# Performance work log

Measured on AMD Instinct MI355X. Metric: run time of the kernel, lower is better.

## Reference

```python
import jax, jax.numpy as jnp
import numpy as np

BATCH, BITS = 1024, 2048
STD = 0.01


def sine_act(x):
    # MySine: 0.5*(1+sin((x-0.5)*pi)), symmetric about 0.5
    return 0.5 * (1.0 + jnp.sin((x - 0.5) * jnp.pi))


def qubo_cost(xb, Q):
    # cost_fn_tensor: per-row QUBO cost c_i = x_i^T Q x_i  -> shape [batch]
    return jnp.einsum('bi,ij,bj->b', xb, Q, xb)


def setup_inputs() -> dict:
    key = jax.random.key(0)
    k1, k2, k3, k4, k5 = jax.random.split(key, 5)
    x = jax.random.uniform(k1, (BATCH, BITS), dtype=jnp.float32)
    noise = jax.random.uniform(k2, (BATCH, BITS), dtype=jnp.float32)  # rand_like in Sample_Binary
    # generate_weights_and_biases: W = I + N(0, std^2), b = N(0, std^2); fc2 gets identical values
    W1 = jnp.eye(BITS, dtype=jnp.float32) + STD * jax.random.normal(k3, (BITS, BITS), dtype=jnp.float32)
    b1 = STD * jax.random.normal(k4, (BITS,), dtype=jnp.float32)
    W2 = W1
    b2 = b1
    # concrete TSP-style QUBO cost matrix (baked into cost_fn in the original repo)
    Q = jax.random.normal(k5, (BITS, BITS), dtype=jnp.float32) / np.float32(BITS)
    return {"x": x, "noise": noise, "W1": W1, "b1": b1, "W2": W2, "b2": b2, "Q": Q}


def reference(x, noise, W1, b1, W2, b2, Q):
    # fc1 + MySine
    h = sine_act(x @ W1.T + b1)
    # fc2 + MySine (layers == 2)
    h = sine_act(h @ W2.T + b2)
    # Sample_Binary: straight-through Bernoulli sample
    sampled = (noise < h).astype(jnp.float32)
    xb = h + jax.lax.stop_gradient(sampled - h)  # numerically exactly 0/1
    # BinaryToCost forward: per-row cost
    return qubo_cost(xb, Q)
```

## Files before the change

### kernel.cpp

```cpp
#include <hip/hip_runtime.h>
#include <math.h>

#define BATCH 1024
#define BITS  2048

typedef __attribute__((ext_vector_type(8))) short bf16x8;
typedef __attribute__((ext_vector_type(4))) float f32x4;
typedef _Float16 f16_t;
typedef __attribute__((ext_vector_type(8))) _Float16 f16x8;

__device__ __constant__ double D_PI = 3.141592653589793;

static __device__ __forceinline__ unsigned short f32_to_bf16(float f) {
    unsigned int u = __float_as_uint(f);
    u += 0x7fffu + ((u >> 16) & 1u);
    return (unsigned short)(u >> 16);
}

__global__ __launch_bounds__(256)
void split_w(const float* __restrict__ W, f16_t* __restrict__ eh, f16_t* __restrict__ el)
{
    const size_t base = ((size_t)blockIdx.x * 256 + threadIdx.x) * 8;
    const int n = (int)(base >> 11);
    const int k0 = (int)(base & 2047);
    float4 w0 = *(const float4*)&W[base];
    float4 w1 = *(const float4*)&W[base + 4];
    float wv[8] = {w0.x, w0.y, w0.z, w0.w, w1.x, w1.y, w1.z, w1.w};
    f16x8 hv, lv;
    #pragma unroll
    for (int j = 0; j < 8; ++j) {
        float e = wv[j] - ((n == k0 + j) ? 1.0f : 0.0f);
        f16_t h = (f16_t)e;
        hv[j] = h;
        lv[j] = (f16_t)((e - (float)h) * 2048.0f);
    }
    *(f16x8*)&eh[base] = hv;
    *(f16x8*)&el[base] = lv;
}

__global__ __launch_bounds__(256)
void split_x(const float* __restrict__ X, f16_t* __restrict__ xh, f16_t* __restrict__ xl)
{
    const size_t base = ((size_t)blockIdx.x * 256 + threadIdx.x) * 8;
    float4 w0 = *(const float4*)&X[base];
    float4 w1 = *(const float4*)&X[base + 4];
    float wv[8] = {w0.x, w0.y, w0.z, w0.w, w1.x, w1.y, w1.z, w1.w};
    f16x8 hv, lv;
    #pragma unroll
    for (int j = 0; j < 8; ++j) {
        f16_t h = (f16_t)wv[j];
        hv[j] = h;
        lv[j] = (f16_t)((wv[j] - (float)h) * 2048.0f);
    }
    *(f16x8*)&xh[base] = hv;
    *(f16x8*)&xl[base] = lv;
}

#define LBM 64
#define LBN 64
#define LBK 64
#define LLS 72

__global__ __launch_bounds__(256)
void layer_mfma(const f16_t* __restrict__ Ah, const f16_t* __restrict__ Al,
                const f16_t* __restrict__ Ebh, const f16_t* __restrict__ Ebl,
                const float* __restrict__ direct, const float* __restrict__ bias,
                const float* __restrict__ noise,
                float* __restrict__ h_f32, f16_t* __restrict__ h_hi,
                f16_t* __restrict__ h_lo, unsigned short* __restrict__ xb_out,
                int mode)
{
    __shared__ __align__(16) f16_t sAh[LBM][LLS], sAl[LBM][LLS];
    __shared__ __align__(16) f16_t sEh[LBN][LLS], sEl[LBN][LLS];

    const int t = threadIdx.x;
    const int wave = t >> 6, lane = t & 63;
    const int quad = lane >> 4, li = lane & 15;
    const int mw = wave & 1, nw = wave >> 1;
    const int row0 = blockIdx.y * LBM, col0 = blockIdx.x * LBN;

    f32x4 acc[2][2][4];
    double acc64[2][2][4];
    #pragma unroll
    for (int tm = 0; tm < 2; ++tm)
        #pragma unroll
        for (int tn = 0; tn < 2; ++tn) {
            #pragma unroll
            for (int p = 0; p < 4; ++p) acc[tm][tn][p] = (f32x4){0.f,0.f,0.f,0.f};
            #pragma unroll
            for (int r = 0; r < 4; ++r) acc64[tm][tn][r] = 0.0;
        }

    const float C1 = 1.0f / 2048.0f;
    const float C2 = 1.0f / (2048.0f * 2048.0f);
    const int srow = t >> 2;
    const int sko  = (t & 3) * 16;

    for (int kt = 0; kt < BITS / LBK; ++kt) {
        const int k0 = kt * LBK;
        {
            const size_t ga = (size_t)(row0 + srow) * BITS + k0 + sko;
            const size_t ge = (size_t)(col0 + srow) * BITS + k0 + sko;
            *(f16x8*)&sAh[srow][sko]     = *(const f16x8*)&Ah[ga];
            *(f16x8*)&sAh[srow][sko + 8] = *(const f16x8*)&Ah[ga + 8];
            *(f16x8*)&sAl[srow][sko]     = *(const f16x8*)&Al[ga];
            *(f16x8*)&sAl[srow][sko + 8] = *(const f16x8*)&Al[ga + 8];
            *(f16x8*)&sEh[srow][sko]     = *(const f16x8*)&Ebh[ge];
            *(f16x8*)&sEh[srow][sko + 8] = *(const f16x8*)&Ebh[ge + 8];
            *(f16x8*)&sEl[srow][sko]     = *(const f16x8*)&Ebl[ge];
            *(f16x8*)&sEl[srow][sko + 8] = *(const f16x8*)&Ebl[ge + 8];
        }
        __syncthreads();

        #pragma unroll
        for (int ks = 0; ks < LBK; ks += 32) {
            f16x8 ah[2], al[2], bh[2], bl[2];
            #pragma unroll
            for (int tm = 0; tm < 2; ++tm) {
                const int r = mw * 32 + tm * 16 + li, c = ks + quad * 8;
                ah[tm] = *(const f16x8*)&sAh[r][c];
                al[tm] = *(const f16x8*)&sAl[r][c];
            }
            #pragma unroll
            for (int tn = 0; tn < 2; ++tn) {
                const int r = nw * 32 + tn * 16 + li, c = ks + quad * 8;
                bh[tn] = *(const f16x8*)&sEh[r][c];
                bl[tn] = *(const f16x8*)&sEl[r][c];
            }
            #pragma unroll
            for (int tm = 0; tm < 2; ++tm)
                #pragma unroll
                for (int tn = 0; tn < 2; ++tn) {
                    acc[tm][tn][0] = __builtin_amdgcn_mfma_f32_16x16x32_f16(ah[tm], bh[tn], acc[tm][tn][0], 0, 0, 0);
                    acc[tm][tn][1] = __builtin_amdgcn_mfma_f32_16x16x32_f16(ah[tm], bl[tn], acc[tm][tn][1], 0, 0, 0);
                    acc[tm][tn][2] = __builtin_amdgcn_mfma_f32_16x16x32_f16(al[tm], bh[tn], acc[tm][tn][2], 0, 0, 0);
                    acc[tm][tn][3] = __builtin_amdgcn_mfma_f32_16x16x32_f16(al[tm], bl[tn], acc[tm][tn][3], 0, 0, 0);
                }
        }
        __syncthreads();

        if ((kt & 7) == 7) {
            #pragma unroll
            for (int tm = 0; tm < 2; ++tm)
                #pragma unroll
                for (int tn = 0; tn < 2; ++tn) {
                    #pragma unroll
                    for (int r = 0; r < 4; ++r) {
                        float s = fmaf(C2, acc[tm][tn][3][r],
                                  fmaf(C1, acc[tm][tn][2][r],
                                  fmaf(C1, acc[tm][tn][1][r], acc[tm][tn][0][r])));
                        acc64[tm][tn][r] += (double)s;
                    }
                    #pragma unroll
                    for (int p = 0; p < 4; ++p) acc[tm][tn][p] = (f32x4){0.f,0.f,0.f,0.f};
                }
        }
    }

    #pragma unroll
    for (int tm = 0; tm < 2; ++tm)
        #pragma unroll
        for (int tn = 0; tn < 2; ++tn)
            #pragma unroll
            for (int r = 0; r < 4; ++r) {
                const int m = row0 + mw * 32 + tm * 16 + quad * 4 + r;
                const int n = col0 + nw * 32 + tn * 16 + li;
                const size_t idx = (size_t)m * BITS + n;
                double pre = acc64[tm][tn][r] + (double)direct[idx] + (double)bias[n];
                double h = 0.5 * (1.0 + sin((pre - 0.5) * D_PI));
                if (mode == 0) {
                    h_f32[idx] = (float)h;
                    f16_t hh = (f16_t)h;
                    h_hi[idx] = hh;
                    h_lo[idx] = (f16_t)((h - (double)hh) * 2048.0);
                } else {
                    xb_out[idx] = ((double)noise[idx] < h) ? (unsigned short)0x3F80
                                                           : (unsigned short)0;
                }
            }
}

__global__ __launch_bounds__(256)
void transpose_q(const float* __restrict__ Q, unsigned short* __restrict__ QT)
{
    __shared__ unsigned short tile[32][33];
    const int t = threadIdx.x;
    const int tx = t & 31, ty = t >> 5;
    const int i0 = blockIdx.y * 32, j0 = blockIdx.x * 32;
    #pragma unroll
    for (int r = 0; r < 4; ++r) {
        const int i = ty + r * 8;
        tile[i][tx] = f32_to_bf16(Q[(size_t)(i0 + i) * BITS + j0 + tx]);
    }
    __syncthreads();
    #pragma unroll
    for (int r = 0; r < 4; ++r) {
        const int j = ty + r * 8;
        QT[(size_t)(j0 + j) * BITS + i0 + tx] = tile[tx][j];
    }
}

#define CBM 64
#define CBN 128
#define CBK 64
#define LSTR (CBK + 8)

__global__ __launch_bounds__(256)
void cost_kernel(const unsigned short* __restrict__ xb,
                 const unsigned short* __restrict__ QT,
                 float* __restrict__ out)
{
    __shared__ unsigned short Ab[CBM][LSTR];
    __shared__ unsigned short Bb[CBN][LSTR];
    __shared__ float red[2][CBM][17];

    const int t = threadIdx.x;
    const int wave = t >> 6, lane = t & 63;
    const int quad = lane >> 4, li = lane & 15;
    const int mw = wave & 1, nw = wave >> 1;
    const int b0 = blockIdx.y * CBM, j0 = blockIdx.x * CBN;

    f32x4 acc[2][4];
    #pragma unroll
    for (int tm = 0; tm < 2; ++tm)
        #pragma unroll
        for (int tn = 0; tn < 4; ++tn)
            acc[tm][tn] = (f32x4){0.f, 0.f, 0.f, 0.f};

    for (int k0 = 0; k0 < BITS; k0 += CBK) {
        #pragma unroll
        for (int i = 0; i < 2; ++i) {
            const int c = t + 256 * i;
            const int row = c >> 3, ko = (c & 7) * 8;
            *(bf16x8*)&Ab[row][ko] =
                *(const bf16x8*)&xb[(size_t)(b0 + row) * BITS + k0 + ko];
        }
        #pragma unroll
        for (int i = 0; i < 4; ++i) {
            const int c = t + 256 * i;
            const int row = c >> 3, ko = (c & 7) * 8;
            *(bf16x8*)&Bb[row][ko] =
                *(const bf16x8*)&QT[(size_t)(j0 + row) * BITS + k0 + ko];
        }
        __syncthreads();

        #pragma unroll
        for (int kk = 0; kk < CBK; kk += 32) {
            bf16x8 af[2], bfr[4];
            #pragma unroll
            for (int tm = 0; tm < 2; ++tm)
                af[tm] = *(const bf16x8*)&Ab[mw * 32 + tm * 16 + li][kk + quad * 8];
            #pragma unroll
            for (int tn = 0; tn < 4; ++tn)
                bfr[tn] = *(const bf16x8*)&Bb[nw * 64 + tn * 16 + li][kk + quad * 8];
            #pragma unroll
            for (int tm = 0; tm < 2; ++tm)
                #pragma unroll
                for (int tn = 0; tn < 4; ++tn)
                    acc[tm][tn] = __builtin_amdgcn_mfma_f32_16x16x32_bf16(
                        af[tm], bfr[tn], acc[tm][tn], 0, 0, 0);
        }
        __syncthreads();
    }

    #pragma unroll
    for (int tm = 0; tm < 2; ++tm) {
        #pragma unroll
        for (int r = 0; r < 4; ++r) {
            const int bl = mw * 32 + tm * 16 + quad * 4 + r;
            const int bg = b0 + bl;
            float p = 0.f;
            #pragma unroll
            for (int tn = 0; tn < 4; ++tn) {
                const int jg = j0 + nw * 64 + tn * 16 + li;
                if (xb[(size_t)bg * BITS + jg])
                    p += acc[tm][tn][r];
            }
            red[nw][bl][li] = p;
        }
    }
    __syncthreads();
    if (t < CBM) {
        float s = 0.f;
        #pragma unroll
        for (int c = 0; c < 16; ++c) s += red[0][t][c] + red[1][t][c];
        atomicAdd(&out[b0 + t], s);
    }
}

__global__ void zero_kernel(float* __restrict__ out, int n)
{
    int i = blockIdx.x * 256 + threadIdx.x;
    if (i < n) out[i] = 0.0f;
}

extern "C" void kernel_launch(void* const* d_in, const int* in_sizes, int n_in,
                              void* d_out, int out_size, void* d_ws, size_t ws_size,
                              hipStream_t stream)
{
    const float* x     = (const float*)d_in[0];
    const float* noise = (const float*)d_in[1];
    const float* W1    = (const float*)d_in[2];
    const float* b1    = (const float*)d_in[3];
    const float* b2    = (const float*)d_in[5];
    const float* Q     = (const float*)d_in[6];
    float* out = (float*)d_out;

    char* w = (char*)d_ws;
    const size_t SZ_W = (size_t)BITS * BITS * 2;
    const size_t SZ_X = (size_t)BATCH * BITS * 2;
    f16_t* eh = (f16_t*)(w);
    f16_t* el = (f16_t*)(w + SZ_W);
    f16_t* xh = (f16_t*)(w + 2 * SZ_W);
    f16_t* xl = (f16_t*)(w + 2 * SZ_W + SZ_X);
    unsigned short* QT = (unsigned short*)(w + 2 * SZ_W);
    f16_t* h1h = (f16_t*)(w + 3 * SZ_W);
    f16_t* h1l = (f16_t*)(w + 3 * SZ_W + SZ_X);
    float* h1f = (float*) (w + 3 * SZ_W + 2 * SZ_X);
    unsigned short* xb = (unsigned short*)(w + 3 * SZ_W + 4 * SZ_X);

    dim3 lgrid(BITS / LBN, BATCH / LBM);
    dim3 tgrid(BITS / 32, BITS / 32);
    dim3 cgrid(BITS / CBN, BATCH / CBM);

    split_w<<<(BITS * BITS / 8 + 255) / 256, 256, 0, stream>>>(W1, eh, el);
    split_x<<<(BATCH * BITS / 8 + 255) / 256, 256, 0, stream>>>(x, xh, xl);
    layer_mfma<<<lgrid, 256, 0, stream>>>(xh, xl, eh, el, x, b1, nullptr,
                                          h1f, h1h, h1l, nullptr, 0);
    transpose_q<<<tgrid, 256, 0, stream>>>(Q, QT);
    layer_mfma<<<lgrid, 256, 0, stream>>>(h1h, h1l, eh, el, h1f, b2, noise,
                                          nullptr, nullptr, nullptr, xb, 1);
    zero_kernel<<<(BATCH + 255) / 256, 256, 0, stream>>>(out, BATCH);
    cost_kernel<<<cgrid, 256, 0, stream>>>(xb, QT, out);
}
```

Measured before the change: 247.3 us.

## Fuse fp16 split conversions into layer GEMM, add split-K waves, merge prep kernels

The separate split_w and split_x kernels are removed. The layer GEMM now reads fp32 A and W directly and does the hi/lo fp16 split, including the identity subtraction, while loading shared memory. The layer kernel uses 512 threads with two K-groups that each handle half of every 128-wide K chunk, then combines them through a shared-memory reduction. The two cross-term MFMAs now share one accumulator. The Q transpose and output zeroing are merged into one prep kernel, and the cost kernel tile is shrunk to 64 columns for more blocks. The W split is now redone per tile and per layer instead of once, trading repeated conversion work and more fp32 global traffic for fewer launches and no intermediate fp16 buffers.

```diff
diff --git a/kernel.cpp b/kernel.cpp
--- a/kernel.cpp
+++ b/kernel.cpp
@@ -17,191 +17,196 @@
     return (unsigned short)(u >> 16);
 }
 
-__global__ __launch_bounds__(256)
-void split_w(const float* __restrict__ W, f16_t* __restrict__ eh, f16_t* __restrict__ el)
-{
-    const size_t base = ((size_t)blockIdx.x * 256 + threadIdx.x) * 8;
-    const int n = (int)(base >> 11);
-    const int k0 = (int)(base & 2047);
-    float4 w0 = *(const float4*)&W[base];
-    float4 w1 = *(const float4*)&W[base + 4];
-    float wv[8] = {w0.x, w0.y, w0.z, w0.w, w1.x, w1.y, w1.z, w1.w};
-    f16x8 hv, lv;
-    #pragma unroll
-    for (int j = 0; j < 8; ++j) {
-        float e = wv[j] - ((n == k0 + j) ? 1.0f : 0.0f);
-        f16_t h = (f16_t)e;
-        hv[j] = h;
-        lv[j] = (f16_t)((e - (float)h) * 2048.0f);
-    }
-    *(f16x8*)&eh[base] = hv;
-    *(f16x8*)&el[base] = lv;
-}
-
-__global__ __launch_bounds__(256)
-void split_x(const float* __restrict__ X, f16_t* __restrict__ xh, f16_t* __restrict__ xl)
-{
-    const size_t base = ((size_t)blockIdx.x * 256 + threadIdx.x) * 8;
-    float4 w0 = *(const float4*)&X[base];
-    float4 w1 = *(const float4*)&X[base + 4];
-    float wv[8] = {w0.x, w0.y, w0.z, w0.w, w1.x, w1.y, w1.z, w1.w};
-    f16x8 hv, lv;
-    #pragma unroll
-    for (int j = 0; j < 8; ++j) {
-        f16_t h = (f16_t)wv[j];
-        hv[j] = h;
-        lv[j] = (f16_t)((wv[j] - (float)h) * 2048.0f);
-    }
-    *(f16x8*)&xh[base] = hv;
-    *(f16x8*)&xl[base] = lv;
-}
-
 #define LBM 64
 #define LBN 64
-#define LBK 64
 #define LLS 72
 
-__global__ __launch_bounds__(256)
-void layer_mfma(const f16_t* __restrict__ Ah, const f16_t* __restrict__ Al,
-                const f16_t* __restrict__ Ebh, const f16_t* __restrict__ Ebl,
-                const float* __restrict__ direct, const float* __restrict__ bias,
-                const float* __restrict__ noise,
-                float* __restrict__ h_f32, f16_t* __restrict__ h_hi,
-                f16_t* __restrict__ h_lo, unsigned short* __restrict__ xb_out,
+__global__ __launch_bounds__(512, 4)
+void layer_mfma(const float* __restrict__ A, const float* __restrict__ W,
+                const float* __restrict__ bias, const float* __restrict__ noise,
+                float* __restrict__ h_out, unsigned short* __restrict__ xb_out,
                 int mode)
 {
-    __shared__ __align__(16) f16_t sAh[LBM][LLS], sAl[LBM][LLS];
-    __shared__ __align__(16) f16_t sEh[LBN][LLS], sEl[LBN][LLS];
+    __shared__ __align__(16) f16_t sA[2][2][LBM][LLS];
+    __shared__ __align__(16) f16_t sE[2][2][LBN][LLS];
 
     const int t = threadIdx.x;
     const int wave = t >> 6, lane = t & 63;
     const int quad = lane >> 4, li = lane & 15;
-    const int mw = wave & 1, nw = wave >> 1;
+    const int kg = wave >> 2;
+    const int sw = wave & 3;
+    const int mw = sw & 1, nw = sw >> 1;
     const int row0 = blockIdx.y * LBM, col0 = blockIdx.x * LBN;
 
-    f32x4 acc[2][2][4];
+    const int srow  = t >> 3;
+    const int skoff = (t & 7) * 8;
+
+    f32x4 acc0[2][2], accm[2][2], acc2[2][2];
     double acc64[2][2][4];
     #pragma unroll
     for (int tm = 0; tm < 2; ++tm)
         #pragma unroll
         for (int tn = 0; tn < 2; ++tn) {
-            #pragma unroll
-            for (int p = 0; p < 4; ++p) acc[tm][tn][p] = (f32x4){0.f,0.f,0.f,0.f};
+            acc0[tm][tn] = (f32x4){0.f,0.f,0.f,0.f};
+            accm[tm][tn] = (f32x4){0.f,0.f,0.f,0.f};
+            acc2[tm][tn] = (f32x4){0.f,0.f,0.f,0.f};
             #pragma unroll
             for (int r = 0; r < 4; ++r) acc64[tm][tn][r] = 0.0;
         }
 
     const float C1 = 1.0f / 2048.0f;
     const float C2 = 1.0f / (2048.0f * 2048.0f);
-    const int srow = t >> 2;
-    const int sko  = (t & 3) * 16;
-
-    for (int kt = 0; kt < BITS / LBK; ++kt) {
-        const int k0 = kt * LBK;
-        {
-            const size_t ga = (size_t)(row0 + srow) * BITS + k0 + sko;
-            const size_t ge = (size_t)(col0 + srow) * BITS + k0 + sko;
-            *(f16x8*)&sAh[srow][sko]     = *(const f16x8*)&Ah[ga];
-            *(f16x8*)&sAh[srow][sko + 8] = *(const f16x8*)&Ah[ga + 8];
-            *(f16x8*)&sAl[srow][sko]     = *(const f16x8*)&Al[ga];
-            *(f16x8*)&sAl[srow][sko + 8] = *(const f16x8*)&Al[ga + 8];
-            *(f16x8*)&sEh[srow][sko]     = *(const f16x8*)&Ebh[ge];
-            *(f16x8*)&sEh[srow][sko + 8] = *(const f16x8*)&Ebh[ge + 8];
-            *(f16x8*)&sEl[srow][sko]     = *(const f16x8*)&Ebl[ge];
-            *(f16x8*)&sEl[srow][sko + 8] = *(const f16x8*)&Ebl[ge + 8];
-        }
-        __syncthreads();
-
-        #pragma unroll
-        for (int ks = 0; ks < LBK; ks += 32) {
+
+    for (int it = 0; it < 16; ++it) {
+        const int kbase = it * 128;
+        #pragma unroll
+        for (int b = 0; b < 2; ++b) {
+            const int kglo = kbase + b * 64 + skoff;
+            {
+                const float* ap = &A[(size_t)(row0 + srow) * BITS + kglo];
+                float4 a0 = *(const float4*)ap;
+                float4 a1 = *(const float4*)(ap + 4);
+                float av[8] = {a0.x,a0.y,a0.z,a0.w,a1.x,a1.y,a1.z,a1.w};
+                f16x8 hv, lv;
+                #pragma unroll
+                for (int j = 0; j < 8; ++j) {
+                    f16_t h = (f16_t)av[j];
+                    hv[j] = h;
+                    lv[j] = (f16_t)((av[j] - (float)h) * 2048.0f);
+                }
+                *(f16x8*)&sA[b][0][srow][skoff] = hv;
+                *(f16x8*)&sA[b][1][srow][skoff] = lv;
+            }
+            {
+                const float* wp = &W[(size_t)(col0 + srow) * BITS + kglo];
+                float4 w0 = *(const float4*)wp;
+                float4 w1 = *(const float4*)(wp + 4);
+                float wv[8] = {w0.x,w0.y,w0.z,w0.w,w1.x,w1.y,w1.z,w1.w};
+                const int diag = (col0 + srow) - kglo;
+                f16x8 hv, lv;
+                #pragma unroll
+                for (int j = 0; j < 8; ++j) {
+                    float e = wv[j] - ((diag == j) ? 1.0f : 0.0f);
+                    f16_t h = (f16_t)e;
+                    hv[j] = h;
+                    lv[j] = (f16_t)((e - (float)h) * 2048.0f);
+                }
+                *(f16x8*)&sE[b][0][srow][skoff] = hv;
+                *(f16x8*)&sE[b][1][srow][skoff] = lv;
+            }
+        }
+        __syncthreads();
+
+        #pragma unroll
+        for (int ks = 0; ks < 64; ks += 32) {
             f16x8 ah[2], al[2], bh[2], bl[2];
+            const int c = ks + quad * 8;
             #pragma unroll
             for (int tm = 0; tm < 2; ++tm) {
-                const int r = mw * 32 + tm * 16 + li, c = ks + quad * 8;
-                ah[tm] = *(const f16x8*)&sAh[r][c];
-                al[tm] = *(const f16x8*)&sAl[r][c];
+                const int r = mw * 32 + tm * 16 + li;
+                ah[tm] = *(const f16x8*)&sA[kg][0][r][c];
+                al[tm] = *(const f16x8*)&sA[kg][1][r][c];
             }
             #pragma unroll
             for (int tn = 0; tn < 2; ++tn) {
-                const int r = nw * 32 + tn * 16 + li, c = ks + quad * 8;
-                bh[tn] = *(const f16x8*)&sEh[r][c];
-                bl[tn] = *(const f16x8*)&sEl[r][c];
+                const int r = nw * 32 + tn * 16 + li;
+                bh[tn] = *(const f16x8*)&sE[kg][0][r][c];
+                bl[tn] = *(const f16x8*)&sE[kg][1][r][c];
             }
             #pragma unroll
             for (int tm = 0; tm < 2; ++tm)
                 #pragma unroll
                 for (int tn = 0; tn < 2; ++tn) {
-                    acc[tm][tn][0] = __builtin_amdgcn_mfma_f32_16x16x32_f16(ah[tm], bh[tn], acc[tm][tn][0], 0, 0, 0);
-                    acc[tm][tn][1] = __builtin_amdgcn_mfma_f32_16x16x32_f16(ah[tm], bl[tn], acc[tm][tn][1], 0, 0, 0);
-                    acc[tm][tn][2] = __builtin_amdgcn_mfma_f32_16x16x32_f16(al[tm], bh[tn], acc[tm][tn][2], 0, 0, 0);
-                    acc[tm][tn][3] = __builtin_amdgcn_mfma_f32_16x16x32_f16(al[tm], bl[tn], acc[tm][tn][3], 0, 0, 0);
-                }
-        }
-        __syncthreads();
-
-        if ((kt & 7) == 7) {
+                    acc0[tm][tn] = __builtin_amdgcn_mfma_f32_16x16x32_f16(ah[tm], bh[tn], acc0[tm][tn], 0, 0, 0);
+                    accm[tm][tn] = __builtin_amdgcn_mfma_f32_16x16x32_f16(al[tm], bh[tn], accm[tm][tn], 0, 0, 0);
+                    accm[tm][tn] = __builtin_amdgcn_mfma_f32_16x16x32_f16(ah[tm], bl[tn], accm[tm][tn], 0, 0, 0);
+                    acc2[tm][tn] = __builtin_amdgcn_mfma_f32_16x16x32_f16(al[tm], bl[tn], acc2[tm][tn], 0, 0, 0);
+                }
+        }
+
+        if ((it & 7) == 7) {
             #pragma unroll
             for (int tm = 0; tm < 2; ++tm)
                 #pragma unroll
                 for (int tn = 0; tn < 2; ++tn) {
                     #pragma unroll
                     for (int r = 0; r < 4; ++r) {
-                        float s = fmaf(C2, acc[tm][tn][3][r],
-                                  fmaf(C1, acc[tm][tn][2][r],
-                                  fmaf(C1, acc[tm][tn][1][r], acc[tm][tn][0][r])));
+                        float s = fmaf(C2, acc2[tm][tn][r],
+                                  fmaf(C1, accm[tm][tn][r], acc0[tm][tn][r]));
                         acc64[tm][tn][r] += (double)s;
                     }
-                    #pragma unroll
-                    for (int p = 0; p < 4; ++p) acc[tm][tn][p] = (f32x4){0.f,0.f,0.f,0.f};
-                }
-        }
-    }
-
-    #pragma unroll
-    for (int tm = 0; tm < 2; ++tm)
-        #pragma unroll
-        for (int tn = 0; tn < 2; ++tn)
-            #pragma unroll
-            for (int r = 0; r < 4; ++r) {
-                const int m = row0 + mw * 32 + tm * 16 + quad * 4 + r;
-                const int n = col0 + nw * 32 + tn * 16 + li;
-                const size_t idx = (size_t)m * BITS + n;
-                double pre = acc64[tm][tn][r] + (double)direct[idx] + (double)bias[n];
-                double h = 0.5 * (1.0 + sin((pre - 0.5) * D_PI));
-                if (mode == 0) {
-                    h_f32[idx] = (float)h;
-                    f16_t hh = (f16_t)h;
-                    h_hi[idx] = hh;
-                    h_lo[idx] = (f16_t)((h - (double)hh) * 2048.0);
-                } else {
-                    xb_out[idx] = ((double)noise[idx] < h) ? (unsigned short)0x3F80
-                                                           : (unsigned short)0;
-                }
-            }
+                    acc0[tm][tn] = (f32x4){0.f,0.f,0.f,0.f};
+                    accm[tm][tn] = (f32x4){0.f,0.f,0.f,0.f};
+                    acc2[tm][tn] = (f32x4){0.f,0.f,0.f,0.f};
+                }
+        }
+        __syncthreads();
+    }
+
+    double* red = (double*)&sA[0][0][0][0];
+    const int rbase = (sw * 64 + lane) * 16;
+    if (kg == 1) {
+        #pragma unroll
+        for (int tm = 0; tm < 2; ++tm)
+            #pragma unroll
+            for (int tn = 0; tn < 2; ++tn)
+                #pragma unroll
+                for (int r = 0; r < 4; ++r)
+                    red[rbase + tm * 8 + tn * 4 + r] = acc64[tm][tn][r];
+    }
+    __syncthreads();
+    if (kg == 0) {
+        #pragma unroll
+        for (int tm = 0; tm < 2; ++tm)
+            #pragma unroll
+            for (int tn = 0; tn < 2; ++tn)
+                #pragma unroll
+                for (int r = 0; r < 4; ++r) {
+                    const int m = row0 + mw * 32 + tm * 16 + quad * 4 + r;
+                    const int n = col0 + nw * 32 + tn * 16 + li;
+                    const size_t idx = (size_t)m * BITS + n;
+                    double pre = acc64[tm][tn][r] + red[rbase + tm * 8 + tn * 4 + r]
+                               + (double)A[idx] + (double)bias[n];
+                    double h = 0.5 * (1.0 + sin((pre - 0.5) * D_PI));
+                    if (mode == 0) {
+                        h_out[idx] = (float)h;
+                    } else {
+                        xb_out[idx] = ((double)noise[idx] < h) ? (unsigned short)0x3F80
+                                                               : (unsigned short)0;
+                    }
+                }
+    }
 }
 
 __global__ __launch_bounds__(256)
-void transpose_q(const float* __restrict__ Q, unsigned short* __restrict__ QT)
+void prep_kernel(const float* __restrict__ Q, unsigned short* __restrict__ QT,
+                 float* __restrict__ out)
 {
     __shared__ unsigned short tile[32][33];
+    const int bid = blockIdx.x;
     const int t = threadIdx.x;
-    const int tx = t & 31, ty = t >> 5;
-    const int i0 = blockIdx.y * 32, j0 = blockIdx.x * 32;
-    #pragma unroll
-    for (int r = 0; r < 4; ++r) {
-        const int i = ty + r * 8;
-        tile[i][tx] = f32_to_bf16(Q[(size_t)(i0 + i) * BITS + j0 + tx]);
-    }
-    __syncthreads();
-    #pragma unroll
-    for (int r = 0; r < 4; ++r) {
-        const int j = ty + r * 8;
-        QT[(size_t)(j0 + j) * BITS + i0 + tx] = tile[tx][j];
+    if (bid < 4096) {
+        const int bx = bid & 63, by = bid >> 6;
+        const int i0 = by * 32, j0 = bx * 32;
+        const int tx = t & 31, ty = t >> 5;
+        #pragma unroll
+        for (int r = 0; r < 4; ++r) {
+            const int i = ty + r * 8;
+            tile[i][tx] = f32_to_bf16(Q[(size_t)(i0 + i) * BITS + j0 + tx]);
+        }
+        __syncthreads();
+        #pragma unroll
+        for (int r = 0; r < 4; ++r) {
+            const int j = ty + r * 8;
+            QT[(size_t)(j0 + j) * BITS + i0 + tx] = tile[tx][j];
+        }
+    } else {
+        *(float4*)&out[t * 4] = (float4){0.f, 0.f, 0.f, 0.f};
     }
 }
 
 #define CBM 64
-#define CBN 128
+#define CBN 64
 #define CBK 64
 #define LSTR (CBK + 8)
 
@@ -220,11 +225,11 @@
     const int mw = wave & 1, nw = wave >> 1;
     const int b0 = blockIdx.y * CBM, j0 = blockIdx.x * CBN;
 
-    f32x4 acc[2][4];
+    f32x4 acc[2][2];
     #pragma unroll
     for (int tm = 0; tm < 2; ++tm)
         #pragma unroll
-        for (int tn = 0; tn < 4; ++tn)
+        for (int tn = 0; tn < 2; ++tn)
             acc[tm][tn] = (f32x4){0.f, 0.f, 0.f, 0.f};
 
     for (int k0 = 0; k0 < BITS; k0 += CBK) {
@@ -234,11 +239,6 @@
             const int row = c >> 3, ko = (c & 7) * 8;
             *(bf16x8*)&Ab[row][ko] =
                 *(const bf16x8*)&xb[(size_t)(b0 + row) * BITS + k0 + ko];
-        }
-        #pragma unroll
-        for (int i = 0; i < 4; ++i) {
-            const int c = t + 256 * i;
-            const int row = c >> 3, ko = (c & 7) * 8;
             *(bf16x8*)&Bb[row][ko] =
                 *(const bf16x8*)&QT[(size_t)(j0 + row) * BITS + k0 + ko];
         }
@@ -246,17 +246,17 @@
 
         #pragma unroll
         for (int kk = 0; kk < CBK; kk += 32) {
-            bf16x8 af[2], bfr[4];
+            bf16x8 af[2], bfr[2];
             #pragma unroll
             for (int tm = 0; tm < 2; ++tm)
                 af[tm] = *(const bf16x8*)&Ab[mw * 32 + tm * 16 + li][kk + quad * 8];
             #pragma unroll
-            for (int tn = 0; tn < 4; ++tn)
-                bfr[tn] = *(const bf16x8*)&Bb[nw * 64 + tn * 16 + li][kk + quad * 8];
+            for (int tn = 0; tn < 2; ++tn)
+                bfr[tn] = *(const bf16x8*)&Bb[nw * 32 + tn * 16 + li][kk + quad * 8];
             #pragma unroll
             for (int tm = 0; tm < 2; ++tm)
                 #pragma unroll
-                for (int tn = 0; tn < 4; ++tn)
+                for (int tn = 0; tn < 2; ++tn)
                     acc[tm][tn] = __builtin_amdgcn_mfma_f32_16x16x32_bf16(
                         af[tm], bfr[tn], acc[tm][tn], 0, 0, 0);
         }
@@ -271,8 +271,8 @@
             const int bg = b0 + bl;
             float p = 0.f;
             #pragma unroll
-            for (int tn = 0; tn < 4; ++tn) {
-                const int jg = j0 + nw * 64 + tn * 16 + li;
+            for (int tn = 0; tn < 2; ++tn) {
+                const int jg = j0 + nw * 32 + tn * 16 + li;
                 if (xb[(size_t)bg * BITS + jg])
                     p += acc[tm][tn][r];
             }
@@ -286,12 +286,6 @@
         for (int c = 0; c < 16; ++c) s += red[0][t][c] + red[1][t][c];
         atomicAdd(&out[b0 + t], s);
     }
-}
-
-__global__ void zero_kernel(float* __restrict__ out, int n)
-{
-    int i = blockIdx.x * 256 + threadIdx.x;
-    if (i < n) out[i] = 0.0f;
 }
 
 extern "C" void kernel_launch(void* const* d_in, const int* in_sizes, int n_in,
@@ -302,34 +296,22 @@
     const float* noise = (const float*)d_in[1];
     const float* W1    = (const float*)d_in[2];
     const float* b1    = (const float*)d_in[3];
+    const float* W2    = (const float*)d_in[4];
     const float* b2    = (const float*)d_in[5];
     const float* Q     = (const float*)d_in[6];
     float* out = (float*)d_out;
 
     char* w = (char*)d_ws;
-    const size_t SZ_W = (size_t)BITS * BITS * 2;
-    const size_t SZ_X = (size_t)BATCH * BITS * 2;
-    f16_t* eh = (f16_t*)(w);
-    f16_t* el = (f16_t*)(w + SZ_W);
-    f16_t* xh = (f16_t*)(w + 2 * SZ_W);
-    f16_t* xl = (f16_t*)(w + 2 * SZ_W + SZ_X);
-    unsigned short* QT = (unsigned short*)(w + 2 * SZ_W);
-    f16_t* h1h = (f16_t*)(w + 3 * SZ_W);
-    f16_t* h1l = (f16_t*)(w + 3 * SZ_W + SZ_X);
-    float* h1f = (float*) (w + 3 * SZ_W + 2 * SZ_X);
-    unsigned short* xb = (unsigned short*)(w + 3 * SZ_W + 4 * SZ_X);
+    unsigned short* QT  = (unsigned short*)(w);
+    float*          h1f = (float*)(w + (size_t)BITS * BITS * 2);
+    unsigned short* xb  = (unsigned short*)(w + (size_t)BITS * BITS * 2
+                                              + (size_t)BATCH * BITS * 4);
 
     dim3 lgrid(BITS / LBN, BATCH / LBM);
-    dim3 tgrid(BITS / 32, BITS / 32);
     dim3 cgrid(BITS / CBN, BATCH / CBM);
 
-    split_w<<<(BITS * BITS / 8 + 255) / 256, 256, 0, stream>>>(W1, eh, el);
-    split_x<<<(BATCH * BITS / 8 + 255) / 256, 256, 0, stream>>>(x, xh, xl);
-    layer_mfma<<<lgrid, 256, 0, stream>>>(xh, xl, eh, el, x, b1, nullptr,
-                                          h1f, h1h, h1l, nullptr, 0);
-    transpose_q<<<tgrid, 256, 0, stream>>>(Q, QT);
-    layer_mfma<<<lgrid, 256, 0, stream>>>(h1h, h1l, eh, el, h1f, b2, noise,
-                                          nullptr, nullptr, nullptr, xb, 1);
-    zero_kernel<<<(BATCH + 255) / 256, 256, 0, stream>>>(out, BATCH);
+    prep_kernel<<<4097, 256, 0, stream>>>(Q, QT, out);
+    layer_mfma<<<lgrid, 512, 0, stream>>>(x,   W1, b1, nullptr, h1f, nullptr, 0);
+    layer_mfma<<<lgrid, 512, 0, stream>>>(h1f, W2, b2, noise,  nullptr, xb, 1);
     cost_kernel<<<cgrid, 256, 0, stream>>>(xb, QT, out);
 }
```

Result: slower. 270.6 us (+9.4%).
